# Kernel optimization log

Hardware: AMD Instinct MI355X
Metric: run time of the kernel (lower is better)

Reference implementation:

```python
import jax, jax.numpy as jnp
import numpy as np

RHO, MU, DT = 1.0, 0.1, 4.0
AX_X, AX_Y = -1, -2  # x = last axis, y = second-to-last


def first_derivative(f, ax, scheme):
    # unit grid spacing; boundary wrap is irrelevant since [1:-1,1:-1] is sliced off
    if scheme == 'left':
        return f - jnp.roll(f, 1, ax)
    if scheme == 'right':
        return jnp.roll(f, -1, ax) - f
    return 0.5 * (jnp.roll(f, -1, ax) - jnp.roll(f, 1, ax))  # central


def vel_map(f, ax, side):
    # staggered-grid interpolation of velocity to neighboring face
    if side == 'left':
        return 0.5 * (f + jnp.roll(f, 1, ax))
    return 0.5 * (f + jnp.roll(f, -1, ax))


def laplacian(f):
    return (jnp.roll(f, 1, AX_X) + jnp.roll(f, -1, AX_X)
            + jnp.roll(f, 1, AX_Y) + jnp.roll(f, -1, AX_Y) - 4.0 * f)


def setup_inputs() -> dict:
    key = jax.random.key(0)
    k1, k2, k3, k4 = jax.random.split(key, 4)
    B, H, W = 8, 1024, 1024
    return {
        'v_old': jax.random.normal(k1, (B, 2, H, W), dtype=jnp.float32),
        'v_new': jax.random.normal(k2, (B, 2, H, W), dtype=jnp.float32),
        'p_new': jax.random.normal(k3, (B, 1, H, W), dtype=jnp.float32),
        'flow_mask_mac': jax.random.randint(k4, (B, 1, H, W), 0, 2).astype(jnp.int32),
    }


def reference(v_old, v_new, p_new, flow_mask_mac):
    mask = flow_mask_mac.astype(v_old.dtype)
    v = 0.5 * (v_new + v_old)  # integration == 'imex'

    u_old, w_old = v_old[:, 0:1], v_old[:, 1:2]
    u_new, w_new = v_new[:, 0:1], v_new[:, 1:2]
    u, w = v[:, 0:1], v[:, 1:2]

    # x-momentum residual (channel 1)
    res_x = mask * (RHO * ((w_new - w_old) / DT
                           + w * first_derivative(w, AX_X, 'central')
                           + 0.5 * (vel_map(u, AX_X, 'left') * first_derivative(w, AX_Y, 'left')
                                    + vel_map(u, AX_X, 'right') * first_derivative(w, AX_Y, 'right')))
                    + first_derivative(p_new, AX_X, 'left')
                    - MU * laplacian(w))

    # y-momentum residual (channel 0)
    res_y = mask * (RHO * ((u_new - u_old) / DT
                           + u * first_derivative(u, AX_Y, 'central')
                           + 0.5 * (vel_map(w, AX_Y, 'left') * first_derivative(u, AX_X, 'left')
                                    + vel_map(w, AX_Y, 'right') * first_derivative(u, AX_X, 'right')))
                    + first_derivative(p_new, AX_Y, 'left')
                    - MU * laplacian(u))

    loss_x = jnp.mean(jnp.square(res_x)[:, :, 1:-1, 1:-1], axis=(1, 2, 3))
    loss_y = jnp.mean(jnp.square(res_y)[:, :, 1:-1, 1:-1], axis=(1, 2, 3))
    return loss_x + loss_y  # shape [B]
```

## Files before the change

kernel.cpp:

```cpp
#include <hip/hip_runtime.h>


#define NS_H 1024
#define NS_W 1024
#define RPB 4
#define NBY 256
#define PARTS_PER_B NBY

__device__ __forceinline__ float4 ld4(const float* p) { return *(const float4*)p; }
__device__ __forceinline__ int4  ld4i(const int* p)   { return *(const int4*)p; }
__device__ __forceinline__ float4 avg4(float4 a, float4 b) {
    return make_float4(0.5f*(a.x+b.x), 0.5f*(a.y+b.y), 0.5f*(a.z+b.z), 0.5f*(a.w+b.w));
}
__device__ __forceinline__ float4 sub4(float4 a, float4 b) {
    return make_float4(a.x-b.x, a.y-b.y, a.z-b.z, a.w-b.w);
}

__global__ __launch_bounds__(512, 3) void ns_loss_partial(
    const float* __restrict__ v_old,
    const float* __restrict__ v_new,
    const float* __restrict__ p,
    const int*   __restrict__ mask,
    float* __restrict__ ws)
{
    const int blkp = blockIdx.x;
    const int lg   = (blkp & 7) * NBY + (blkp >> 3);
    const int b    = lg / NBY;
    const int cy   = lg % NBY;
    const int y0   = 1 + cy * RPB;

    const size_t hw = (size_t)NS_H * NS_W;
    const float* uo = v_old + (size_t)b * 2 * hw;
    const float* wo = uo + hw;
    const float* un = v_new + (size_t)b * 2 * hw;
    const float* wn = un + hw;
    const float* pb = p    + (size_t)b * hw;
    const int*   mb = mask + (size_t)b * hw;

    const int tid  = (int)threadIdx.x;
    const int h    = tid >> 8;
    const int t    = tid & 255;
    const int lane = tid & 63;
    const int wid  = tid >> 6;
    const int wih  = (t >> 6);
    const int x0   = t * 4;
    const bool has_r = (t != 255);

    const int y = y0 + h * 2;

    int Rm = y - 1, Rc = y, Rp = y + 1, Rq = y + 2;
    if (Rc > 1023) Rc = 1023;
    if (Rp > 1023) Rp = 1023;
    if (Rq > 1023) Rq = 1023;
    const float rv_c = (y     <= NS_H - 2) ? 1.f : 0.f;
    const float rv_p = (y + 1 <= NS_H - 2) ? 1.f : 0.f;

    const int rm  = Rm * NS_W;
    const int rc  = Rc * NS_W;
    const int rp  = Rp * NS_W;
    const int rpp = Rq * NS_W;

    float4 un_m = ld4(un + rm  + x0), uo_m = ld4(uo + rm  + x0);
    float4 un_c = ld4(un + rc  + x0), uo_c = ld4(uo + rc  + x0);
    float4 un_p = ld4(un + rp  + x0), uo_p = ld4(uo + rp  + x0);
    float4 un_q = ld4(un + rpp + x0), uo_q = ld4(uo + rpp + x0);
    float4 wn_m = ld4(wn + rm  + x0), wo_m = ld4(wo + rm  + x0);
    float4 wn_c = ld4(wn + rc  + x0), wo_c = ld4(wo + rc  + x0);
    float4 wn_p = ld4(wn + rp  + x0), wo_p = ld4(wo + rp  + x0);
    float4 wn_q = ld4(wn + rpp + x0), wo_q = ld4(wo + rpp + x0);
    float4 p_m4 = ld4(pb + rm + x0);
    float4 p_c4 = ld4(pb + rc + x0);
    float4 p_p4 = ld4(pb + rp + x0);
    int4   m_c4 = ld4i(mb + rc + x0);
    int4   m_p4 = ld4i(mb + rp + x0);
    __builtin_amdgcn_sched_barrier(0);

    float4 u_m = avg4(un_m, uo_m), u_c = avg4(un_c, uo_c);
    float4 u_p = avg4(un_p, uo_p), u_q = avg4(un_q, uo_q);
    float4 w_m = avg4(wn_m, wo_m), w_c = avg4(wn_c, wo_c);
    float4 w_p = avg4(wn_p, wo_p), w_q = avg4(wn_q, wo_q);
    float4 du_c = sub4(un_c, uo_c), du_p = sub4(un_p, uo_p);
    float4 dw_c = sub4(wn_c, wo_c), dw_p = sub4(wn_p, wo_p);

    __shared__ float edge[8][10];
    if (lane == 63) {
        edge[wid][0] = u_c.w;  edge[wid][1] = w_c.w;  edge[wid][2] = p_c4.w;
        edge[wid][3] = u_p.w;  edge[wid][4] = w_p.w;  edge[wid][5] = p_p4.w;
    }
    if (lane == 0) {
        edge[wid][6] = u_c.x;  edge[wid][7] = w_c.x;
        edge[wid][8] = u_p.x;  edge[wid][9] = w_p.x;
    }
    __syncthreads();

    float ul_c = __shfl_up(u_c.w, 1),  wl_c = __shfl_up(w_c.w, 1);
    float ul_p = __shfl_up(u_p.w, 1),  wl_p = __shfl_up(w_p.w, 1);
    float pl_c = __shfl_up(p_c4.w, 1), pl_p = __shfl_up(p_p4.w, 1);
    if (lane == 0 && wih > 0) {
        ul_c = edge[wid-1][0]; wl_c = edge[wid-1][1]; pl_c = edge[wid-1][2];
        ul_p = edge[wid-1][3]; wl_p = edge[wid-1][4]; pl_p = edge[wid-1][5];
    }
    float ur_c = __shfl_down(u_c.x, 1), wr_c = __shfl_down(w_c.x, 1);
    float ur_p = __shfl_down(u_p.x, 1), wr_p = __shfl_down(w_p.x, 1);
    if (lane == 63 && wih < 3) {
        ur_c = edge[wid+1][6]; wr_c = edge[wid+1][7];
        ur_p = edge[wid+1][8]; wr_p = edge[wid+1][9];
    }
    if (!has_r) { ur_c = 0.f; wr_c = 0.f; ur_p = 0.f; wr_p = 0.f; }

    float acc = 0.f;

    {
        const float uc[6]  = {ul_c, u_c.x, u_c.y, u_c.z, u_c.w, ur_c};
        const float wcv[6] = {wl_c, w_c.x, w_c.y, w_c.z, w_c.w, wr_c};
        const float uym[4] = {u_m.x, u_m.y, u_m.z, u_m.w};
        const float uyp[4] = {u_p.x, u_p.y, u_p.z, u_p.w};
        const float wym[4] = {w_m.x, w_m.y, w_m.z, w_m.w};
        const float wyp[4] = {w_p.x, w_p.y, w_p.z, w_p.w};
        const float du[4]  = {du_c.x, du_c.y, du_c.z, du_c.w};
        const float dw[4]  = {dw_c.x, dw_c.y, dw_c.z, dw_c.w};
        const float pcv[5] = {pl_c, p_c4.x, p_c4.y, p_c4.z, p_c4.w};
        const float pym[4] = {p_m4.x, p_m4.y, p_m4.z, p_m4.w};
        const int   mm[4]  = {m_c4.x, m_c4.y, m_c4.z, m_c4.w};

        #pragma unroll
        for (int j = 0; j < 4; ++j) {
            const int x = x0 + j;
            const float m = ((x >= 1 && x <= NS_W - 2) ? (float)mm[j] : 0.f) * rv_c;
            const float u_cc = uc[j+1],  u_xm = uc[j],  u_xp = uc[j+2];
            const float w_cc = wcv[j+1], w_xm = wcv[j], w_xp = wcv[j+2];

            float res_x =
                dw[j] * 0.25f
              + w_cc * 0.5f * (w_xp - w_xm)
              + 0.5f * ( 0.5f * (u_cc + u_xm) * (w_cc   - wym[j])
                       + 0.5f * (u_cc + u_xp) * (wyp[j] - w_cc  ) )
              + (pcv[j+1] - pcv[j])
              - 0.1f * (w_xm + w_xp + wym[j] + wyp[j] - 4.f * w_cc);

            float res_y =
                du[j] * 0.25f
              + u_cc * 0.5f * (uyp[j] - uym[j])
              + 0.5f * ( 0.5f * (w_cc + wym[j]) * (u_cc - u_xm)
                       + 0.5f * (w_cc + wyp[j]) * (u_xp - u_cc) )
              + (pcv[j+1] - pym[j])
              - 0.1f * (u_xm + u_xp + uym[j] + uyp[j] - 4.f * u_cc);

            acc += m * (res_x * res_x + res_y * res_y);
        }
    }

    {
        const float uc[6]  = {ul_p, u_p.x, u_p.y, u_p.z, u_p.w, ur_p};
        const float wcv[6] = {wl_p, w_p.x, w_p.y, w_p.z, w_p.w, wr_p};
        const float uym[4] = {u_c.x, u_c.y, u_c.z, u_c.w};
        const float uyp[4] = {u_q.x, u_q.y, u_q.z, u_q.w};
        const float wym[4] = {w_c.x, w_c.y, w_c.z, w_c.w};
        const float wyp[4] = {w_q.x, w_q.y, w_q.z, w_q.w};
        const float du[4]  = {du_p.x, du_p.y, du_p.z, du_p.w};
        const float dw[4]  = {dw_p.x, dw_p.y, dw_p.z, dw_p.w};
        const float pcv[5] = {pl_p, p_p4.x, p_p4.y, p_p4.z, p_p4.w};
        const float pym[4] = {p_c4.x, p_c4.y, p_c4.z, p_c4.w};
        const int   mm[4]  = {m_p4.x, m_p4.y, m_p4.z, m_p4.w};

        #pragma unroll
        for (int j = 0; j < 4; ++j) {
            const int x = x0 + j;
            const float m = ((x >= 1 && x <= NS_W - 2) ? (float)mm[j] : 0.f) * rv_p;
            const float u_cc = uc[j+1],  u_xm = uc[j],  u_xp = uc[j+2];
            const float w_cc = wcv[j+1], w_xm = wcv[j], w_xp = wcv[j+2];

            float res_x =
                dw[j] * 0.25f
              + w_cc * 0.5f * (w_xp - w_xm)
              + 0.5f * ( 0.5f * (u_cc + u_xm) * (w_cc   - wym[j])
                       + 0.5f * (u_cc + u_xp) * (wyp[j] - w_cc  ) )
              + (pcv[j+1] - pcv[j])
              - 0.1f * (w_xm + w_xp + wym[j] + wyp[j] - 4.f * w_cc);

            float res_y =
                du[j] * 0.25f
              + u_cc * 0.5f * (uyp[j] - uym[j])
              + 0.5f * ( 0.5f * (w_cc + wym[j]) * (u_cc - u_xm)
                       + 0.5f * (w_cc + wyp[j]) * (u_xp - u_cc) )
              + (pcv[j+1] - pym[j])
              - 0.1f * (u_xm + u_xp + uym[j] + uyp[j] - 4.f * u_cc);

            acc += m * (res_x * res_x + res_y * res_y);
        }
    }

    #pragma unroll
    for (int off = 32; off > 0; off >>= 1)
        acc += __shfl_down(acc, off);

    __shared__ float smem[8];
    if (lane == 0) smem[wid] = acc;
    __syncthreads();

    if (tid == 0)
        ws[lg] = smem[0] + smem[1] + smem[2] + smem[3]
               + smem[4] + smem[5] + smem[6] + smem[7];
}

__global__ __launch_bounds__(256) void ns_loss_reduce(
    const float* __restrict__ ws, float* __restrict__ out)
{
    const int b = blockIdx.x;
    float acc = 0.f;
    for (int i = threadIdx.x; i < PARTS_PER_B; i += 256)
        acc += ws[b * PARTS_PER_B + i];

    #pragma unroll
    for (int off = 32; off > 0; off >>= 1)
        acc += __shfl_down(acc, off);

    __shared__ float smem[4];
    const int lane = threadIdx.x & 63;
    const int wid  = threadIdx.x >> 6;
    if (lane == 0) smem[wid] = acc;
    __syncthreads();

    if (threadIdx.x == 0) {
        const float inv = 1.0f / ((float)(NS_H - 2) * (float)(NS_W - 2));
        out[b] = (smem[0] + smem[1] + smem[2] + smem[3]) * inv;
    }
}

extern "C" void kernel_launch(void* const* d_in, const int* in_sizes, int n_in,
                              void* d_out, int out_size, void* d_ws, size_t ws_size,
                              hipStream_t stream) {
    const float* v_old = (const float*)d_in[0];
    const float* v_new = (const float*)d_in[1];
    const float* p_new = (const float*)d_in[2];
    const int*   msk   = (const int*)d_in[3];
    float* out = (float*)d_out;
    float* ws  = (float*)d_ws;

    const int B = out_size;

    ns_loss_partial<<<dim3(B * NBY), dim3(512), 0, stream>>>(v_old, v_new, p_new, msk, ws);
    ns_loss_reduce<<<dim3(B), dim3(256), 0, stream>>>(ws, out);
}
```

Before: 200.0 us.

## Share overlapping halo rows between half-blocks through LDS instead of reloading

```diff
diff --git a/kernel.cpp b/kernel.cpp
--- a/kernel.cpp
+++ b/kernel.cpp
@@ -5,6 +5,7 @@
 #define NS_W 1024
 #define RPB 4
 #define NBY 256
+#define NBLK (8 * NBY)
 #define PARTS_PER_B NBY
 
 __device__ __forceinline__ float4 ld4(const float* p) { return *(const float4*)p; }
@@ -14,6 +15,43 @@
 }
 __device__ __forceinline__ float4 sub4(float4 a, float4 b) {
     return make_float4(a.x-b.x, a.y-b.y, a.z-b.z, a.w-b.w);
+}
+
+__device__ __forceinline__ float row_stencil(
+    const float uc[6], const float wcv[6],
+    const float uym[4], const float uyp[4],
+    const float wym[4], const float wyp[4],
+    const float du[4], const float dw[4],
+    const float pcv[5], const float pym[4],
+    const int mm[4], int xbase, float rv)
+{
+    float acc = 0.f;
+    #pragma unroll
+    for (int j = 0; j < 4; ++j) {
+        const int x = xbase + j;
+        const float m = ((x >= 1 && x <= NS_W - 2) ? (float)mm[j] : 0.f) * rv;
+        const float u_cc = uc[j+1],  u_xm = uc[j],  u_xp = uc[j+2];
+        const float w_cc = wcv[j+1], w_xm = wcv[j], w_xp = wcv[j+2];
+
+        float res_x =
+            dw[j] * 0.25f
+          + w_cc * 0.5f * (w_xp - w_xm)
+          + 0.5f * ( 0.5f * (u_cc + u_xm) * (w_cc   - wym[j])
+                   + 0.5f * (u_cc + u_xp) * (wyp[j] - w_cc  ) )
+          + (pcv[j+1] - pcv[j])
+          - 0.1f * (w_xm + w_xp + wym[j] + wyp[j] - 4.f * w_cc);
+
+        float res_y =
+            du[j] * 0.25f
+          + u_cc * 0.5f * (uyp[j] - uym[j])
+          + 0.5f * ( 0.5f * (w_cc + wym[j]) * (u_cc - u_xm)
+                   + 0.5f * (w_cc + wyp[j]) * (u_xp - u_cc) )
+          + (pcv[j+1] - pym[j])
+          - 0.1f * (u_xm + u_xp + uym[j] + uyp[j] - 4.f * u_cc);
+
+        acc += m * (res_x * res_x + res_y * res_y);
+    }
+    return acc;
 }
 
 __global__ __launch_bounds__(512, 3) void ns_loss_partial(
@@ -25,8 +63,8 @@
 {
     const int blkp = blockIdx.x;
     const int lg   = (blkp & 7) * NBY + (blkp >> 3);
-    const int b    = lg / NBY;
-    const int cy   = lg % NBY;
+    const int b    = lg >> 8;
+    const int cy   = lg & 255;
     const int y0   = 1 + cy * RPB;
 
     const size_t hw = (size_t)NS_H * NS_W;
@@ -41,152 +79,190 @@
     const int h    = tid >> 8;
     const int t    = tid & 255;
     const int lane = tid & 63;
-    const int wid  = tid >> 6;
-    const int wih  = (t >> 6);
-    const int x0   = t * 4;
-    const bool has_r = (t != 255);
-
-    const int y = y0 + h * 2;
-
-    int Rm = y - 1, Rc = y, Rp = y + 1, Rq = y + 2;
-    if (Rc > 1023) Rc = 1023;
-    if (Rp > 1023) Rp = 1023;
-    if (Rq > 1023) Rq = 1023;
-    const float rv_c = (y     <= NS_H - 2) ? 1.f : 0.f;
-    const float rv_p = (y + 1 <= NS_H - 2) ? 1.f : 0.f;
-
-    const int rm  = Rm * NS_W;
-    const int rc  = Rc * NS_W;
-    const int rp  = Rp * NS_W;
-    const int rpp = Rq * NS_W;
-
-    float4 un_m = ld4(un + rm  + x0), uo_m = ld4(uo + rm  + x0);
-    float4 un_c = ld4(un + rc  + x0), uo_c = ld4(uo + rc  + x0);
-    float4 un_p = ld4(un + rp  + x0), uo_p = ld4(uo + rp  + x0);
-    float4 un_q = ld4(un + rpp + x0), uo_q = ld4(uo + rpp + x0);
-    float4 wn_m = ld4(wn + rm  + x0), wo_m = ld4(wo + rm  + x0);
-    float4 wn_c = ld4(wn + rc  + x0), wo_c = ld4(wo + rc  + x0);
-    float4 wn_p = ld4(wn + rp  + x0), wo_p = ld4(wo + rp  + x0);
-    float4 wn_q = ld4(wn + rpp + x0), wo_q = ld4(wo + rpp + x0);
-    float4 p_m4 = ld4(pb + rm + x0);
-    float4 p_c4 = ld4(pb + rc + x0);
-    float4 p_p4 = ld4(pb + rp + x0);
-    int4   m_c4 = ld4i(mb + rc + x0);
-    int4   m_p4 = ld4i(mb + rp + x0);
-    __builtin_amdgcn_sched_barrier(0);
-
-    float4 u_m = avg4(un_m, uo_m), u_c = avg4(un_c, uo_c);
-    float4 u_p = avg4(un_p, uo_p), u_q = avg4(un_q, uo_q);
-    float4 w_m = avg4(wn_m, wo_m), w_c = avg4(wn_c, wo_c);
-    float4 w_p = avg4(wn_p, wo_p), w_q = avg4(wn_q, wo_q);
-    float4 du_c = sub4(un_c, uo_c), du_p = sub4(un_p, uo_p);
-    float4 dw_c = sub4(wn_c, wo_c), dw_p = sub4(wn_p, wo_p);
-
-    __shared__ float edge[8][10];
-    if (lane == 63) {
-        edge[wid][0] = u_c.w;  edge[wid][1] = w_c.w;  edge[wid][2] = p_c4.w;
-        edge[wid][3] = u_p.w;  edge[wid][4] = w_p.w;  edge[wid][5] = p_p4.w;
-    }
-    if (lane == 0) {
-        edge[wid][6] = u_c.x;  edge[wid][7] = w_c.x;
-        edge[wid][8] = u_p.x;  edge[wid][9] = w_p.x;
-    }
-    __syncthreads();
-
-    float ul_c = __shfl_up(u_c.w, 1),  wl_c = __shfl_up(w_c.w, 1);
-    float ul_p = __shfl_up(u_p.w, 1),  wl_p = __shfl_up(w_p.w, 1);
-    float pl_c = __shfl_up(p_c4.w, 1), pl_p = __shfl_up(p_p4.w, 1);
-    if (lane == 0 && wih > 0) {
-        ul_c = edge[wid-1][0]; wl_c = edge[wid-1][1]; pl_c = edge[wid-1][2];
-        ul_p = edge[wid-1][3]; wl_p = edge[wid-1][4]; pl_p = edge[wid-1][5];
-    }
-    float ur_c = __shfl_down(u_c.x, 1), wr_c = __shfl_down(w_c.x, 1);
-    float ur_p = __shfl_down(u_p.x, 1), wr_p = __shfl_down(w_p.x, 1);
-    if (lane == 63 && wih < 3) {
-        ur_c = edge[wid+1][6]; wr_c = edge[wid+1][7];
-        ur_p = edge[wid+1][8]; wr_p = edge[wid+1][9];
-    }
-    if (!has_r) { ur_c = 0.f; wr_c = 0.f; ur_p = 0.f; wr_p = 0.f; }
+    const int q0   = t * 4;
+    const bool seamL = (lane == 0)  && (q0 > 0);
+    const bool seamR = (lane == 63) && (q0 + 4 < NS_W);
+
+    const int rm = (y0 - 1) * NS_W;
+    const int rc = rm + NS_W;
+    const int rp = rc + NS_W;
+    const int rq = rp + NS_W;
+    int Rr = y0 + 3; if (Rr > 1023) Rr = 1023;
+    int Rs = y0 + 4; if (Rs > 1023) Rs = 1023;
+    const int rr = Rr * NS_W;
+    const int rs = Rs * NS_W;
+    const float rv_q = (y0 + 2 <= NS_H - 2) ? 1.f : 0.f;
+    const float rv_r = (y0 + 3 <= NS_H - 2) ? 1.f : 0.f;
+
+    __shared__ float shr[7][1024];
+    __shared__ float sred[8];
 
     float acc = 0.f;
 
-    {
-        const float uc[6]  = {ul_c, u_c.x, u_c.y, u_c.z, u_c.w, ur_c};
-        const float wcv[6] = {wl_c, w_c.x, w_c.y, w_c.z, w_c.w, wr_c};
-        const float uym[4] = {u_m.x, u_m.y, u_m.z, u_m.w};
-        const float uyp[4] = {u_p.x, u_p.y, u_p.z, u_p.w};
-        const float wym[4] = {w_m.x, w_m.y, w_m.z, w_m.w};
-        const float wyp[4] = {w_p.x, w_p.y, w_p.z, w_p.w};
-        const float du[4]  = {du_c.x, du_c.y, du_c.z, du_c.w};
-        const float dw[4]  = {dw_c.x, dw_c.y, dw_c.z, dw_c.w};
-        const float pcv[5] = {pl_c, p_c4.x, p_c4.y, p_c4.z, p_c4.w};
-        const float pym[4] = {p_m4.x, p_m4.y, p_m4.z, p_m4.w};
-        const int   mm[4]  = {m_c4.x, m_c4.y, m_c4.z, m_c4.w};
-
-        #pragma unroll
-        for (int j = 0; j < 4; ++j) {
-            const int x = x0 + j;
-            const float m = ((x >= 1 && x <= NS_W - 2) ? (float)mm[j] : 0.f) * rv_c;
-            const float u_cc = uc[j+1],  u_xm = uc[j],  u_xp = uc[j+2];
-            const float w_cc = wcv[j+1], w_xm = wcv[j], w_xp = wcv[j+2];
-
-            float res_x =
-                dw[j] * 0.25f
-              + w_cc * 0.5f * (w_xp - w_xm)
-              + 0.5f * ( 0.5f * (u_cc + u_xm) * (w_cc   - wym[j])
-                       + 0.5f * (u_cc + u_xp) * (wyp[j] - w_cc  ) )
-              + (pcv[j+1] - pcv[j])
-              - 0.1f * (w_xm + w_xp + wym[j] + wyp[j] - 4.f * w_cc);
-
-            float res_y =
-                du[j] * 0.25f
-              + u_cc * 0.5f * (uyp[j] - uym[j])
-              + 0.5f * ( 0.5f * (w_cc + wym[j]) * (u_cc - u_xm)
-                       + 0.5f * (w_cc + wyp[j]) * (u_xp - u_cc) )
-              + (pcv[j+1] - pym[j])
-              - 0.1f * (u_xm + u_xp + uym[j] + uyp[j] - 4.f * u_cc);
-
-            acc += m * (res_x * res_x + res_y * res_y);
-        }
-    }
-
-    {
-        const float uc[6]  = {ul_p, u_p.x, u_p.y, u_p.z, u_p.w, ur_p};
-        const float wcv[6] = {wl_p, w_p.x, w_p.y, w_p.z, w_p.w, wr_p};
-        const float uym[4] = {u_c.x, u_c.y, u_c.z, u_c.w};
-        const float uyp[4] = {u_q.x, u_q.y, u_q.z, u_q.w};
-        const float wym[4] = {w_c.x, w_c.y, w_c.z, w_c.w};
-        const float wyp[4] = {w_q.x, w_q.y, w_q.z, w_q.w};
-        const float du[4]  = {du_p.x, du_p.y, du_p.z, du_p.w};
-        const float dw[4]  = {dw_p.x, dw_p.y, dw_p.z, dw_p.w};
-        const float pcv[5] = {pl_p, p_p4.x, p_p4.y, p_p4.z, p_p4.w};
-        const float pym[4] = {p_c4.x, p_c4.y, p_c4.z, p_c4.w};
-        const int   mm[4]  = {m_p4.x, m_p4.y, m_p4.z, m_p4.w};
-
-        #pragma unroll
-        for (int j = 0; j < 4; ++j) {
-            const int x = x0 + j;
-            const float m = ((x >= 1 && x <= NS_W - 2) ? (float)mm[j] : 0.f) * rv_p;
-            const float u_cc = uc[j+1],  u_xm = uc[j],  u_xp = uc[j+2];
-            const float w_cc = wcv[j+1], w_xm = wcv[j], w_xp = wcv[j+2];
-
-            float res_x =
-                dw[j] * 0.25f
-              + w_cc * 0.5f * (w_xp - w_xm)
-              + 0.5f * ( 0.5f * (u_cc + u_xm) * (w_cc   - wym[j])
-                       + 0.5f * (u_cc + u_xp) * (wyp[j] - w_cc  ) )
-              + (pcv[j+1] - pcv[j])
-              - 0.1f * (w_xm + w_xp + wym[j] + wyp[j] - 4.f * w_cc);
-
-            float res_y =
-                du[j] * 0.25f
-              + u_cc * 0.5f * (uyp[j] - uym[j])
-              + 0.5f * ( 0.5f * (w_cc + wym[j]) * (u_cc - u_xm)
-                       + 0.5f * (w_cc + wyp[j]) * (u_xp - u_cc) )
-              + (pcv[j+1] - pym[j])
-              - 0.1f * (u_xm + u_xp + uym[j] + uyp[j] - 4.f * u_cc);
-
-            acc += m * (res_x * res_x + res_y * res_y);
+    if (h == 0) {
+        float4 un_m = ld4(un + rm + q0), uo_m = ld4(uo + rm + q0);
+        float4 un_c = ld4(un + rc + q0), uo_c = ld4(uo + rc + q0);
+        float4 un_p = ld4(un + rp + q0), uo_p = ld4(uo + rp + q0);
+        float4 un_q = ld4(un + rq + q0), uo_q = ld4(uo + rq + q0);
+        float4 wn_m = ld4(wn + rm + q0), wo_m = ld4(wo + rm + q0);
+        float4 wn_c = ld4(wn + rc + q0), wo_c = ld4(wo + rc + q0);
+        float4 wn_p = ld4(wn + rp + q0), wo_p = ld4(wo + rp + q0);
+        float4 wn_q = ld4(wn + rq + q0), wo_q = ld4(wo + rq + q0);
+        float4 p_m4 = ld4(pb + rm + q0);
+        float4 p_c4 = ld4(pb + rc + q0);
+        float4 p_p4 = ld4(pb + rp + q0);
+        int4   m_c4 = ld4i(mb + rc + q0);
+        int4   m_p4 = ld4i(mb + rp + q0);
+
+        float sulc = 0.f, swlc = 0.f, splc = 0.f, sulp = 0.f, swlp = 0.f, splp = 0.f;
+        float surc = 0.f, swrc = 0.f, surp = 0.f, swrp = 0.f;
+        if (seamL) {
+            sulc = 0.5f * (un[rc + q0 - 1] + uo[rc + q0 - 1]);
+            swlc = 0.5f * (wn[rc + q0 - 1] + wo[rc + q0 - 1]);
+            splc = pb[rc + q0 - 1];
+            sulp = 0.5f * (un[rp + q0 - 1] + uo[rp + q0 - 1]);
+            swlp = 0.5f * (wn[rp + q0 - 1] + wo[rp + q0 - 1]);
+            splp = pb[rp + q0 - 1];
+        }
+        if (seamR) {
+            surc = 0.5f * (un[rc + q0 + 4] + uo[rc + q0 + 4]);
+            swrc = 0.5f * (wn[rc + q0 + 4] + wo[rc + q0 + 4]);
+            surp = 0.5f * (un[rp + q0 + 4] + uo[rp + q0 + 4]);
+            swrp = 0.5f * (wn[rp + q0 + 4] + wo[rp + q0 + 4]);
+        }
+        __builtin_amdgcn_sched_barrier(0);
+
+        float4 u_m = avg4(un_m, uo_m), u_c = avg4(un_c, uo_c);
+        float4 u_p = avg4(un_p, uo_p), u_q = avg4(un_q, uo_q);
+        float4 w_m = avg4(wn_m, wo_m), w_c = avg4(wn_c, wo_c);
+        float4 w_p = avg4(wn_p, wo_p), w_q = avg4(wn_q, wo_q);
+        float4 du_c = sub4(un_c, uo_c), du_p = sub4(un_p, uo_p);
+        float4 dw_c = sub4(wn_c, wo_c), dw_p = sub4(wn_p, wo_p);
+        float4 du_q = sub4(un_q, uo_q), dw_q = sub4(wn_q, wo_q);
+
+        *(float4*)&shr[0][q0] = u_p;  *(float4*)&shr[1][q0] = w_p;
+        *(float4*)&shr[2][q0] = u_q;  *(float4*)&shr[3][q0] = w_q;
+        *(float4*)&shr[4][q0] = du_q; *(float4*)&shr[5][q0] = dw_q;
+        *(float4*)&shr[6][q0] = p_p4;
+        __builtin_amdgcn_sched_barrier(0);
+        asm volatile("s_waitcnt lgkmcnt(0)" ::: "memory");
+        __builtin_amdgcn_s_barrier();
+        __builtin_amdgcn_sched_barrier(0);
+
+        float ul_c = __shfl_up(u_c.w, 1),  wl_c = __shfl_up(w_c.w, 1);
+        float ul_p = __shfl_up(u_p.w, 1),  wl_p = __shfl_up(w_p.w, 1);
+        float pl_c = __shfl_up(p_c4.w, 1), pl_p = __shfl_up(p_p4.w, 1);
+        if (lane == 0) { ul_c = sulc; wl_c = swlc; pl_c = splc;
+                         ul_p = sulp; wl_p = swlp; pl_p = splp; }
+        float ur_c = __shfl_down(u_c.x, 1), wr_c = __shfl_down(w_c.x, 1);
+        float ur_p = __shfl_down(u_p.x, 1), wr_p = __shfl_down(w_p.x, 1);
+        if (lane == 63) { ur_c = surc; wr_c = swrc; ur_p = surp; wr_p = swrp; }
+
+        {
+            const float uc[6]  = {ul_c, u_c.x, u_c.y, u_c.z, u_c.w, ur_c};
+            const float wcv[6] = {wl_c, w_c.x, w_c.y, w_c.z, w_c.w, wr_c};
+            const float uym[4] = {u_m.x, u_m.y, u_m.z, u_m.w};
+            const float uyp[4] = {u_p.x, u_p.y, u_p.z, u_p.w};
+            const float wym[4] = {w_m.x, w_m.y, w_m.z, w_m.w};
+            const float wyp[4] = {w_p.x, w_p.y, w_p.z, w_p.w};
+            const float du[4]  = {du_c.x, du_c.y, du_c.z, du_c.w};
+            const float dw[4]  = {dw_c.x, dw_c.y, dw_c.z, dw_c.w};
+            const float pcv[5] = {pl_c, p_c4.x, p_c4.y, p_c4.z, p_c4.w};
+            const float pym[4] = {p_m4.x, p_m4.y, p_m4.z, p_m4.w};
+            const int   mm[4]  = {m_c4.x, m_c4.y, m_c4.z, m_c4.w};
+            acc += row_stencil(uc, wcv, uym, uyp, wym, wyp, du, dw, pcv, pym, mm, q0, 1.f);
+        }
+        {
+            const float uc[6]  = {ul_p, u_p.x, u_p.y, u_p.z, u_p.w, ur_p};
+            const float wcv[6] = {wl_p, w_p.x, w_p.y, w_p.z, w_p.w, wr_p};
+            const float uym[4] = {u_c.x, u_c.y, u_c.z, u_c.w};
+            const float uyp[4] = {u_q.x, u_q.y, u_q.z, u_q.w};
+            const float wym[4] = {w_c.x, w_c.y, w_c.z, w_c.w};
+            const float wyp[4] = {w_q.x, w_q.y, w_q.z, w_q.w};
+            const float du[4]  = {du_p.x, du_p.y, du_p.z, du_p.w};
+            const float dw[4]  = {dw_p.x, dw_p.y, dw_p.z, dw_p.w};
+            const float pcv[5] = {pl_p, p_p4.x, p_p4.y, p_p4.z, p_p4.w};
+            const float pym[4] = {p_c4.x, p_c4.y, p_c4.z, p_c4.w};
+            const int   mm[4]  = {m_p4.x, m_p4.y, m_p4.z, m_p4.w};
+            acc += row_stencil(uc, wcv, uym, uyp, wym, wyp, du, dw, pcv, pym, mm, q0, 1.f);
+        }
+    } else {
+        float4 un_r = ld4(un + rr + q0), uo_r = ld4(uo + rr + q0);
+        float4 wn_r = ld4(wn + rr + q0), wo_r = ld4(wo + rr + q0);
+        float4 un_s = ld4(un + rs + q0), uo_s = ld4(uo + rs + q0);
+        float4 wn_s = ld4(wn + rs + q0), wo_s = ld4(wo + rs + q0);
+        float4 p_q4 = ld4(pb + rq + q0);
+        float4 p_r4 = ld4(pb + rr + q0);
+        int4   m_q4 = ld4i(mb + rq + q0);
+        int4   m_r4 = ld4i(mb + rr + q0);
+
+        float sulr = 0.f, swlr = 0.f, splr = 0.f, splq = 0.f;
+        float surr = 0.f, swrr = 0.f;
+        if (seamL) {
+            sulr = 0.5f * (un[rr + q0 - 1] + uo[rr + q0 - 1]);
+            swlr = 0.5f * (wn[rr + q0 - 1] + wo[rr + q0 - 1]);
+            splr = pb[rr + q0 - 1];
+            splq = pb[rq + q0 - 1];
+        }
+        if (seamR) {
+            surr = 0.5f * (un[rr + q0 + 4] + uo[rr + q0 + 4]);
+            swrr = 0.5f * (wn[rr + q0 + 4] + wo[rr + q0 + 4]);
+        }
+        __builtin_amdgcn_sched_barrier(0);
+        __builtin_amdgcn_s_barrier();
+        __builtin_amdgcn_sched_barrier(0);
+
+        const int il = (q0 > 0) ? q0 - 1 : 0;
+        const int ir = (q0 + 4 < NS_W) ? q0 + 4 : NS_W - 1;
+        float4 u_p4 = *(const float4*)&shr[0][q0];
+        float4 w_p4 = *(const float4*)&shr[1][q0];
+        float4 u_q4 = *(const float4*)&shr[2][q0];
+        float4 w_q4 = *(const float4*)&shr[3][q0];
+        float4 duq4 = *(const float4*)&shr[4][q0];
+        float4 dwq4 = *(const float4*)&shr[5][q0];
+        float4 pp4  = *(const float4*)&shr[6][q0];
+        const float ul_q = shr[2][il], ur_q = shr[2][ir];
+        const float wl_q = shr[3][il], wr_q = shr[3][ir];
+
+        float4 u_r = avg4(un_r, uo_r), w_r = avg4(wn_r, wo_r);
+        float4 du_r = sub4(un_r, uo_r), dw_r = sub4(wn_r, wo_r);
+        float4 u_s = avg4(un_s, uo_s), w_s = avg4(wn_s, wo_s);
+
+        float pl_q = __shfl_up(p_q4.w, 1);
+        if (lane == 0) pl_q = splq;
+        float ul_r = __shfl_up(u_r.w, 1),  wl_r = __shfl_up(w_r.w, 1);
+        float pl_r = __shfl_up(p_r4.w, 1);
+        if (lane == 0) { ul_r = sulr; wl_r = swlr; pl_r = splr; }
+        float ur_r = __shfl_down(u_r.x, 1), wr_r = __shfl_down(w_r.x, 1);
+        if (lane == 63) { ur_r = surr; wr_r = swrr; }
+
+        {
+            const float uc[6]  = {ul_q, u_q4.x, u_q4.y, u_q4.z, u_q4.w, ur_q};
+            const float wcv[6] = {wl_q, w_q4.x, w_q4.y, w_q4.z, w_q4.w, wr_q};
+            const float uym[4] = {u_p4.x, u_p4.y, u_p4.z, u_p4.w};
+            const float uyp[4] = {u_r.x, u_r.y, u_r.z, u_r.w};
+            const float wym[4] = {w_p4.x, w_p4.y, w_p4.z, w_p4.w};
+            const float wyp[4] = {w_r.x, w_r.y, w_r.z, w_r.w};
+            const float du[4]  = {duq4.x, duq4.y, duq4.z, duq4.w};
+            const float dw[4]  = {dwq4.x, dwq4.y, dwq4.z, dwq4.w};
+            const float pcv[5] = {pl_q, p_q4.x, p_q4.y, p_q4.z, p_q4.w};
+            const float pym[4] = {pp4.x, pp4.y, pp4.z, pp4.w};
+            const int   mm[4]  = {m_q4.x, m_q4.y, m_q4.z, m_q4.w};
+            acc += row_stencil(uc, wcv, uym, uyp, wym, wyp, du, dw, pcv, pym, mm, q0, rv_q);
+        }
+        {
+            const float uc[6]  = {ul_r, u_r.x, u_r.y, u_r.z, u_r.w, ur_r};
+            const float wcv[6] = {wl_r, w_r.x, w_r.y, w_r.z, w_r.w, wr_r};
+            const float uym[4] = {u_q4.x, u_q4.y, u_q4.z, u_q4.w};
+            const float uyp[4] = {u_s.x, u_s.y, u_s.z, u_s.w};
+            const float wym[4] = {w_q4.x, w_q4.y, w_q4.z, w_q4.w};
+            const float wyp[4] = {w_s.x, w_s.y, w_s.z, w_s.w};
+            const float du[4]  = {du_r.x, du_r.y, du_r.z, du_r.w};
+            const float dw[4]  = {dw_r.x, dw_r.y, dw_r.z, dw_r.w};
+            const float pcv[5] = {pl_r, p_r4.x, p_r4.y, p_r4.z, p_r4.w};
+            const float pym[4] = {p_q4.x, p_q4.y, p_q4.z, p_q4.w};
+            const int   mm[4]  = {m_r4.x, m_r4.y, m_r4.z, m_r4.w};
+            acc += row_stencil(uc, wcv, uym, uyp, wym, wyp, du, dw, pcv, pym, mm, q0, rv_r);
         }
     }
 
@@ -194,13 +270,15 @@
     for (int off = 32; off > 0; off >>= 1)
         acc += __shfl_down(acc, off);
 
-    __shared__ float smem[8];
-    if (lane == 0) smem[wid] = acc;
+    if (lane == 0) sred[tid >> 6] = acc;
     __syncthreads();
 
-    if (tid == 0)
-        ws[lg] = smem[0] + smem[1] + smem[2] + smem[3]
-               + smem[4] + smem[5] + smem[6] + smem[7];
+    if (tid == 0) {
+        float s = 0.f;
+        #pragma unroll
+        for (int i = 0; i < 8; ++i) s += sred[i];
+        ws[lg] = s;
+    }
 }
 
 __global__ __launch_bounds__(256) void ns_loss_reduce(
@@ -237,8 +315,6 @@
     float* out = (float*)d_out;
     float* ws  = (float*)d_ws;
 
-    const int B = out_size;
-
-    ns_loss_partial<<<dim3(B * NBY), dim3(512), 0, stream>>>(v_old, v_new, p_new, msk, ws);
-    ns_loss_reduce<<<dim3(B), dim3(256), 0, stream>>>(ws, out);
-}
+    ns_loss_partial<<<dim3(NBLK), dim3(512), 0, stream>>>(v_old, v_new, p_new, msk, ws);
+    ns_loss_reduce<<<dim3(8), dim3(256), 0, stream>>>(ws, out);
+}
```

After: 211.2 us. 1.06x slower.
